# Kernel tuning notes

Measured on AMD Instinct MI355X. Metric: run time of the kernel, lower is better.

## Reference

```python
import jax, jax.numpy as jnp
import numpy as np

N, T = 64, 256
TOTAL_NODES, C_IN = 25, 128          # c = 3200
NUM_SEEDS, C_OUT = 5, 3              # seeds flat dim = 15
NEW_NODES = 20
LIN_IN = TOTAL_NODES * C_IN + NUM_SEEDS * C_OUT  # 3215


def setup_inputs() -> dict:
    key = jax.random.key(0)
    k1, k2, k3 = jax.random.split(key, 3)
    x = jax.random.normal(k1, (N, T, TOTAL_NODES * C_IN), dtype=jnp.float32)
    seeds = jax.random.normal(k2, (N, T, NUM_SEEDS, C_OUT), dtype=jnp.float32)
    # Stacked weights of the `new_nodes` cloned Linear(LIN_IN, C_OUT) layers.
    W = jax.random.normal(k3, (NEW_NODES, C_OUT, LIN_IN), dtype=jnp.float32) * 0.02
    b = jnp.zeros((NEW_NODES, C_OUT), dtype=jnp.float32)
    return {"x": x, "seeds": seeds, "W": W, "b": b}


def reference(x, seeds, W, b):
    n, t, _ = x.shape
    mix = jnp.concatenate([x, seeds.reshape(n, t, -1)], axis=2)  # [n,t,LIN_IN]
    # Fuse all cloned small Linears into one batched GEMM, then layout as
    # torch.stack([...], dim=3): output [n, t, c_out, new_nodes].
    out = jnp.einsum('ntc,koc->ntok', mix, W) + b.T  # b.T: [c_out, new_nodes]
    return out
```

## Files before the change

### kernel.cpp

```cpp
#include <hip/hip_runtime.h>


#define NROWS    16384
#define CIN      3200
#define SEED_K   15
#define LIN_IN   3215
#define NCOL     60
#define KB_MAIN  100
#define KB_TOT   101
#define WB_ELEMS (KB_TOT * 4 * 64 * 8)
#define CHUNK_KB 2
#define NCHUNKS  50
#define A_BYTES  1024
#define B_BASE   16384
#define SMEM_SZ  32768

typedef __attribute__((ext_vector_type(8))) __bf16 bf16x8;
typedef __attribute__((ext_vector_type(4))) float f32x4;
typedef __attribute__((ext_vector_type(8))) unsigned short ushort8;

__device__ unsigned short Wb_g[WB_ELEMS];
__device__ __align__(16) float bias_g[64];

__device__ inline unsigned short f2bf_rne(float f) {
    unsigned int u = __builtin_bit_cast(unsigned int, f);
    u += 0x7fffu + ((u >> 16) & 1u);
    return (unsigned short)(u >> 16);
}

__device__ inline bf16x8 to_bf16x8(f32x4 a0, f32x4 a1) {
    ushort8 u;
    u[0] = f2bf_rne(a0[0]); u[1] = f2bf_rne(a0[1]);
    u[2] = f2bf_rne(a0[2]); u[3] = f2bf_rne(a0[3]);
    u[4] = f2bf_rne(a1[0]); u[5] = f2bf_rne(a1[1]);
    u[6] = f2bf_rne(a1[2]); u[7] = f2bf_rne(a1[2 + 1]);
    return __builtin_bit_cast(bf16x8, u);
}

typedef __attribute__((address_space(3))) void lds_void;
typedef __attribute__((address_space(1))) const void gm_void;
__device__ __forceinline__ void gll16(const void* g, void* l) {
    __builtin_amdgcn_global_load_lds((gm_void*)g, (lds_void*)l, 16, 0, 0);
}

__global__ void prep_B(const float* __restrict__ W, const float* __restrict__ b) {
    int idx = blockIdx.x * blockDim.x + threadIdx.x;
    if (idx >= WB_ELEMS) return;
    if (idx < 64) bias_g[idx] = (idx < NCOL) ? b[(idx % 20) * 3 + (idx / 20)] : 0.f;
    int jj   = idx & 7;
    int lane = (idx >> 3) & 63;
    int nt   = (idx >> 9) & 3;
    int kb   = idx >> 11;
    int k = kb * 32 + (lane >> 4) * 8 + jj;
    int n = nt * 16 + (lane & 15);
    float v = 0.0f;
    if (k < LIN_IN && n < NCOL) {
        int o = n / 20, kn = n % 20;
        v = W[(kn * 3 + o) * LIN_IN + k];
    }
    Wb_g[idx] = f2bf_rne(v);
}

__global__ __launch_bounds__(256) void gen_nodes(
    const float* __restrict__ x, const float* __restrict__ seeds,
    float* __restrict__ out) {
    const int lane = threadIdx.x & 63;
    const int wave = threadIdx.x >> 6;
    const int quad = lane >> 4;
    const int l15  = lane & 15;
    const int rb0  = blockIdx.x * 32;
    const int wt   = wave & 1;
    const int nh   = wave >> 1;

    __shared__ __align__(16) char smem[SMEM_SZ];

    const float* xlane = x + (size_t)(rb0 + l15) * CIN + quad * 8;

    f32x4 acc[2];
    acc[0] = (f32x4){0.f, 0.f, 0.f, 0.f};
    acc[1] = (f32x4){0.f, 0.f, 0.f, 0.f};

    auto stage = [&](int c, int buf) {
        if (wave < 2) {
            const int kb  = wave;
            const int cbk = c * CHUNK_KB + kb;
            const float* s0 = xlane + (size_t)cbk * 32;
            char* ab = smem + ((buf * 2 + kb) * 4) * A_BYTES;
            gll16(s0,                ab);
            gll16(s0 + 4,            ab + 1024);
            gll16(s0 + 16 * CIN,     ab + 2048);
            gll16(s0 + 16 * CIN + 4, ab + 3072);
        } else {
            const int kb  = wave - 2;
            const int cbk = c * CHUNK_KB + kb;
            const unsigned short* s = Wb_g + (size_t)cbk * 2048 + lane * 8;
            char* bb = smem + B_BASE + ((buf * 2 + kb) * 4) * A_BYTES;
            gll16(s,        bb);
            gll16(s + 512,  bb + 1024);
            gll16(s + 1024, bb + 2048);
            gll16(s + 1536, bb + 3072);
        }
    };

    stage(0, 0);
    __syncthreads();

    for (int c = 0; c < NCHUNKS; ++c) {
        const int buf = c & 1;
        if (c + 1 < NCHUNKS) stage(c + 1, buf ^ 1);

#pragma unroll
        for (int kb = 0; kb < CHUNK_KB; ++kb) {
            const char* ab = smem + (((buf * 2 + kb) * 2 + wt) * 2) * A_BYTES + lane * 16;
            f32x4 a0 = *(const f32x4*)(ab);
            f32x4 a1 = *(const f32x4*)(ab + 1024);
            const char* bb = smem + B_BASE + ((buf * 2 + kb) * 4 + nh * 2) * A_BYTES + lane * 16;
            bf16x8 b0 = *(const bf16x8*)(bb);
            bf16x8 b1 = *(const bf16x8*)(bb + 1024);
            bf16x8 af = to_bf16x8(a0, a1);
            acc[0] = __builtin_amdgcn_mfma_f32_16x16x32_bf16(af, b0, acc[0], 0, 0, 0);
            acc[1] = __builtin_amdgcn_mfma_f32_16x16x32_bf16(af, b1, acc[1], 0, 0, 0);
        }
        __syncthreads();
    }

    {
        const float* srow = seeds + (size_t)(rb0 + wt * 16 + l15) * SEED_K;
        f32x4 s0 = {0.f, 0.f, 0.f, 0.f}, s1 = {0.f, 0.f, 0.f, 0.f};
#pragma unroll
        for (int j = 0; j < 4; ++j) {
            int cc = quad * 8 + j;
            if (cc < SEED_K) s0[j] = srow[cc];
            if (cc + 4 < SEED_K) s1[j] = srow[cc + 4];
        }
        bf16x8 af = to_bf16x8(s0, s1);
        const unsigned short* bb = Wb_g + (size_t)KB_MAIN * 2048 + lane * 8;
        bf16x8 b0 = *(const bf16x8*)(bb + nh * 1024);
        bf16x8 b1 = *(const bf16x8*)(bb + nh * 1024 + 512);
        acc[0] = __builtin_amdgcn_mfma_f32_16x16x32_bf16(af, b0, acc[0], 0, 0, 0);
        acc[1] = __builtin_amdgcn_mfma_f32_16x16x32_bf16(af, b1, acc[1], 0, 0, 0);
    }

#pragma unroll
    for (int t = 0; t < 2; ++t) {
        int j = (nh * 2 + t) * 16 + l15;
        if (j < NCOL) {
            float bias = bias_g[j];
#pragma unroll
            for (int r = 0; r < 4; ++r) {
                int m = wt * 16 + quad * 4 + r;
                out[(size_t)(rb0 + m) * NCOL + j] = acc[t][r] + bias;
            }
        }
    }
}

extern "C" void kernel_launch(void* const* d_in, const int* in_sizes, int n_in,
                              void* d_out, int out_size, void* d_ws, size_t ws_size,
                              hipStream_t stream) {
    const float* x     = (const float*)d_in[0];
    const float* seeds = (const float*)d_in[1];
    const float* W     = (const float*)d_in[2];
    const float* b     = (const float*)d_in[3];
    float* out = (float*)d_out;
    (void)d_ws; (void)ws_size;

    prep_B<<<(WB_ELEMS + 255) / 256, 256, 0, stream>>>(W, b);
    gen_nodes<<<NROWS / 32, 256, 0, stream>>>(x, seeds, out);
}
```

Baseline: 298.0 us.

## Deepen LDS prefetch pipeline to six stages with vmcnt-based barriers

Replaces the two-buffer, two-k-block-per-chunk staging with an 8-slot ring and a prefetch depth of 6 k-blocks. All four waves now issue the A and B global-to-LDS loads. Synchronisation uses explicit s_waitcnt vmcnt plus s_barrier in place of __syncthreads. The goal is to keep more memory requests in flight for this bandwidth-bound x stream. In exchange, LDS use doubles to 64KB, which may limit occupancy, and the hand-counted vmcnt values must match the number of outstanding loads exactly.

```diff
diff --git a/kernel.cpp b/kernel.cpp
--- a/kernel.cpp
+++ b/kernel.cpp
@@ -7,13 +7,12 @@
 #define LIN_IN   3215
 #define NCOL     60
 #define KB_MAIN  100
-#define KB_TOT   101
-#define WB_ELEMS (KB_TOT * 4 * 64 * 8)
-#define CHUNK_KB 2
-#define NCHUNKS  50
-#define A_BYTES  1024
-#define B_BASE   16384
-#define SMEM_SZ  32768
+#define WB_ELEMS ((KB_MAIN + 1) * 4 * 64 * 8)
+#define NCHUNKS  100
+#define DEPTH    6
+#define SLOT_SZ  4096
+#define B_BASE   32768
+#define SMEM_SZ  65536
 
 typedef __attribute__((ext_vector_type(8))) __bf16 bf16x8;
 typedef __attribute__((ext_vector_type(4))) float f32x4;
@@ -33,7 +32,7 @@
     u[0] = f2bf_rne(a0[0]); u[1] = f2bf_rne(a0[1]);
     u[2] = f2bf_rne(a0[2]); u[3] = f2bf_rne(a0[3]);
     u[4] = f2bf_rne(a1[0]); u[5] = f2bf_rne(a1[1]);
-    u[6] = f2bf_rne(a1[2]); u[7] = f2bf_rne(a1[2 + 1]);
+    u[6] = f2bf_rne(a1[2]); u[7] = f2bf_rne(a1[3]);
     return __builtin_bit_cast(bf16x8, u);
 }
 
@@ -42,6 +41,8 @@
 __device__ __forceinline__ void gll16(const void* g, void* l) {
     __builtin_amdgcn_global_load_lds((gm_void*)g, (lds_void*)l, 16, 0, 0);
 }
+
+#define VB(N) asm volatile("s_waitcnt vmcnt(" #N ")\n\ts_barrier" ::: "memory")
 
 __global__ void prep_B(const float* __restrict__ W, const float* __restrict__ b) {
     int idx = blockIdx.x * blockDim.x + threadIdx.x;
@@ -74,54 +75,48 @@
 
     __shared__ __align__(16) char smem[SMEM_SZ];
 
-    const float* xlane = x + (size_t)(rb0 + l15) * CIN + quad * 8;
+    const float* aSrc = x + (size_t)(rb0 + (wave >> 1) * 16 + l15) * CIN
+                          + quad * 8 + (wave & 1) * 4;
+    const unsigned short* bSrc = Wb_g + wave * 512 + lane * 8;
 
     f32x4 acc[2];
     acc[0] = (f32x4){0.f, 0.f, 0.f, 0.f};
     acc[1] = (f32x4){0.f, 0.f, 0.f, 0.f};
 
-    auto stage = [&](int c, int buf) {
-        if (wave < 2) {
-            const int kb  = wave;
-            const int cbk = c * CHUNK_KB + kb;
-            const float* s0 = xlane + (size_t)cbk * 32;
-            char* ab = smem + ((buf * 2 + kb) * 4) * A_BYTES;
-            gll16(s0,                ab);
-            gll16(s0 + 4,            ab + 1024);
-            gll16(s0 + 16 * CIN,     ab + 2048);
-            gll16(s0 + 16 * CIN + 4, ab + 3072);
-        } else {
-            const int kb  = wave - 2;
-            const int cbk = c * CHUNK_KB + kb;
-            const unsigned short* s = Wb_g + (size_t)cbk * 2048 + lane * 8;
-            char* bb = smem + B_BASE + ((buf * 2 + kb) * 4) * A_BYTES;
-            gll16(s,        bb);
-            gll16(s + 512,  bb + 1024);
-            gll16(s + 1024, bb + 2048);
-            gll16(s + 1536, bb + 3072);
-        }
+    auto stage = [&](int cbk) {
+        int slot = cbk & 7;
+        gll16(aSrc + (size_t)cbk * 32, smem + slot * SLOT_SZ + wave * 1024);
+        gll16(bSrc + (size_t)cbk * 2048,
+              smem + B_BASE + slot * SLOT_SZ + wave * 1024);
     };
 
-    stage(0, 0);
-    __syncthreads();
+#pragma unroll
+    for (int c0 = 0; c0 < DEPTH; ++c0) stage(c0);
 
     for (int c = 0; c < NCHUNKS; ++c) {
-        const int buf = c & 1;
-        if (c + 1 < NCHUNKS) stage(c + 1, buf ^ 1);
+        if (c + DEPTH < NCHUNKS) {
+            stage(c + DEPTH);
+            VB(12);
+        } else {
+            int ah = NCHUNKS - 1 - c;
+            if      (ah >= 5) VB(10);
+            else if (ah == 4) VB(8);
+            else if (ah == 3) VB(6);
+            else if (ah == 2) VB(4);
+            else if (ah == 1) VB(2);
+            else              VB(0);
+        }
 
-#pragma unroll
-        for (int kb = 0; kb < CHUNK_KB; ++kb) {
-            const char* ab = smem + (((buf * 2 + kb) * 2 + wt) * 2) * A_BYTES + lane * 16;
-            f32x4 a0 = *(const f32x4*)(ab);
-            f32x4 a1 = *(const f32x4*)(ab + 1024);
-            const char* bb = smem + B_BASE + ((buf * 2 + kb) * 4 + nh * 2) * A_BYTES + lane * 16;
-            bf16x8 b0 = *(const bf16x8*)(bb);
-            bf16x8 b1 = *(const bf16x8*)(bb + 1024);
-            bf16x8 af = to_bf16x8(a0, a1);
-            acc[0] = __builtin_amdgcn_mfma_f32_16x16x32_bf16(af, b0, acc[0], 0, 0, 0);
-            acc[1] = __builtin_amdgcn_mfma_f32_16x16x32_bf16(af, b1, acc[1], 0, 0, 0);
-        }
-        __syncthreads();
+        const int slot = c & 7;
+        const char* ab = smem + slot * SLOT_SZ + wt * 2048 + lane * 16;
+        f32x4 a0 = *(const f32x4*)(ab);
+        f32x4 a1 = *(const f32x4*)(ab + 1024);
+        const char* bb = smem + B_BASE + slot * SLOT_SZ + nh * 2048 + lane * 16;
+        bf16x8 b0 = *(const bf16x8*)(bb);
+        bf16x8 b1 = *(const bf16x8*)(bb + 1024);
+        bf16x8 af = to_bf16x8(a0, a1);
+        acc[0] = __builtin_amdgcn_mfma_f32_16x16x32_bf16(af, b0, acc[0], 0, 0, 0);
+        acc[1] = __builtin_amdgcn_mfma_f32_16x16x32_bf16(af, b1, acc[1], 0, 0, 0);
     }
 
     {
```

New measurement: 299.3 us. About the same (+0.4%).
